# Performance work log

Measured on AMD Instinct MI355X. Metric: run time of the kernel, lower is better.

## Reference

```python
import jax, jax.numpy as jnp
import numpy as np

B, XDIM, TWIN, INCH = 1024, 62, 10, 128
MID, OUT, K, K1, LIN, HC = 256, 512, 3, 10, 512, 4
EPS = 1e-5

REGIONS = [
    list(range(0, 5)),
    list(range(5, 8)) + list(range(14, 17)),
    list(range(8, 11)) + list(range(17, 20)),
    list(range(11, 14)) + list(range(20, 23)),
    list(range(23, 26)) + list(range(32, 35)),
    list(range(26, 29)) + list(range(35, 38)),
    list(range(29, 32)) + list(range(38, 41)),
    list(range(41, 44)) + list(range(50, 52)) + list(range(57, 58)),
    list(range(44, 47)) + list(range(52, 55)) + list(range(58, 61)),
    list(range(47, 50)) + list(range(55, 57)) + list(range(61, 62)),
]


def setup_inputs() -> dict:
    key = jax.random.key(0)
    ks = jax.random.split(key, 40)
    n = lambda k, s, sc=0.02: jax.random.normal(k, s, jnp.float32) * sc
    inp = {
        "x": jax.random.normal(ks[0], (B, XDIM, TWIN, INCH), jnp.float32),
        "tfe_w": n(ks[1], (XDIM, TWIN)),          # depthwise Conv2d (10,1) weight, squeezed
        "tfe_b": jnp.zeros((XDIM,), jnp.float32),
        "cheby1_w": n(ks[2], (K, INCH, OUT)),
        "A": n(ks[3], (XDIM, XDIM)),
        "cheby2_w": n(ks[4], (K, MID, OUT)),
        "A1": n(ks[5], (K1, K1)),
        "b_gate": jnp.float32(1.0),
        "c_gate": jnp.float32(1.0),
        "region_b": jnp.zeros((K1, MID), jnp.float32),
        "hc_w1": n(ks[6], (OUT * 72, LIN)),
        "hc_b1": jnp.zeros((LIN,), jnp.float32),
        "bn1_g": jnp.ones((LIN,), jnp.float32),
        "bn1_b": jnp.zeros((LIN,), jnp.float32),
        "hc_w2": n(ks[7], (LIN, LIN // 2)),
        "hc_b2": jnp.zeros((LIN // 2,), jnp.float32),
        "bn2_g": jnp.ones((LIN // 2,), jnp.float32),
        "bn2_b": jnp.zeros((LIN // 2,), jnp.float32),
        "hc_w3": n(ks[8], (LIN // 2, HC)),
        "hc_b3": jnp.zeros((HC,), jnp.float32),
    }
    for i, idx in enumerate(REGIONS):
        inp[f"rw{i+1}"] = n(ks[10 + i], (MID, INCH, len(idx)))
    return inp


def _cheby(x, L, Ws):
    # sum_k  S_k @ x @ W_k  with S_0 = I, S_k = S_{k-1} @ L ; then ReLU
    S = jnp.eye(L.shape[0], dtype=x.dtype)
    res = jnp.zeros(x.shape[:2] + (Ws.shape[-1],), x.dtype)
    for k in range(Ws.shape[0]):
        res = res + jnp.einsum("nm,bmt,to->bno", S, x, Ws[k])
        S = S @ L
    return jax.nn.relu(res)


def _bn(h, g, b):
    mu = h.mean(axis=0)
    v = h.var(axis=0)  # biased, training-mode BatchNorm1d
    return (h - mu) * jax.lax.rsqrt(v + EPS) * g + b


def _forward(x, tfe_w, tfe_b, cheby1_w, A, cheby2_w, A1, b_gate, c_gate,
             rw1, rw2, rw3, rw4, rw5, rw6, rw7, rw8, rw9, rw10, region_b,
             hc_w1, hc_b1, bn1_g, bn1_b, hc_w2, hc_b2, bn2_g, bn2_b, hc_w3, hc_b3):
    # variance gate (torch.var default: unbiased)
    sigma = jnp.var(x, axis=2, ddof=1)                              # (B, 62, INCH)
    g_tfe = jnp.einsum("bcit,ci->bct", x, tfe_w) + tfe_b[None, :, None]
    g = g_tfe * jnp.exp(-sigma)                                      # (B, 62, INCH)

    g1 = _cheby(g, A, cheby1_w)                                      # (B, 62, OUT)

    rws = [rw1, rw2, rw3, rw4, rw5, rw6, rw7, rw8, rw9, rw10]
    RG = []
    for i, (idx, w) in enumerate(zip(REGIONS, rws)):
        reg = g[:, jnp.asarray(idx), :]                              # (B, L, INCH)
        RG.append(jnp.einsum("blc,mcl->bm", reg, w) + region_b[i])   # Conv1d, full-width kernel
    g2in = jnp.stack(RG, axis=1)                                     # (B, 10, MID)
    g2 = _cheby(g2in, A1, cheby2_w)                                  # (B, 10, OUT)

    att = jnp.concatenate([b_gate * g1, c_gate * g2], axis=1)        # (B, 72, OUT)
    cat = jnp.concatenate([g1, g2], axis=1)
    out = jax.nn.softmax(att, axis=1) * cat
    out = out.reshape(out.shape[0], -1)                              # (B, 72*OUT)

    h = jax.nn.gelu(_bn(out @ hc_w1 + hc_b1, bn1_g, bn1_b), approximate=False)
    h = jax.nn.gelu(_bn(h @ hc_w2 + hc_b2, bn2_g, bn2_b), approximate=False)
    h = h @ hc_w3 + hc_b3
    return jax.nn.softmax(h, axis=1)


def reference(x, tfe_w, tfe_b, cheby1_w, A, cheby2_w, A1, b_gate, c_gate,
              rw1, rw2, rw3, rw4, rw5, rw6, rw7, rw8, rw9, rw10, region_b,
              hc_w1, hc_b1, bn1_g, bn1_b, hc_w2, hc_b2, bn2_g, bn2_b, hc_w3, hc_b3):
    return _forward(x, tfe_w, tfe_b, cheby1_w, A, cheby2_w, A1, b_gate, c_gate,
                    rw1, rw2, rw3, rw4, rw5, rw6, rw7, rw8, rw9, rw10, region_b,
                    hc_w1, hc_b1, bn1_g, bn1_b, hc_w2, hc_b2, bn2_g, bn2_b, hc_w3, hc_b3)
```

## Files before the change

### kernel.cpp

```cpp
#include <hip/hip_runtime.h>
#include <math.h>


__constant__ int cOrder[62] = {
  0,1,2,3,4,
  5,6,7,14,15,16,
  8,9,10,17,18,19,
  11,12,13,20,21,22,
  23,24,25,32,33,34,
  26,27,28,35,36,37,
  29,30,31,38,39,40,
  41,42,43,50,51,57,
  44,45,46,52,53,54,58,59,60,
  47,48,49,55,56,61
};
__constant__ int cPos[62] = {
  0,1,2,3,4, 5,6,7, 11,12,13, 17,18,19, 8,9,10, 14,15,16, 20,21,22,
  23,24,25, 29,30,31, 35,36,37, 26,27,28, 32,33,34, 38,39,40,
  41,42,43, 47,48,49, 56,57,58, 44,45, 50,51,52, 59,60, 46, 53,54,55, 61
};
__constant__ int cRegK[10]   = {640,768,768,768,768,768,768,768,1152,768};
__constant__ int cRegCum[10] = {0,640,1408,2176,2944,3712,4480,5248,6016,7168};

struct Ptr10 { const float* p[10]; };

typedef __attribute__((ext_vector_type(8))) short bf16x8;
typedef __attribute__((ext_vector_type(4))) float f32x4;

__device__ __forceinline__ float gelu_exact(float v){
  return 0.5f * v * (1.0f + erff(v * 0.70710678118654752f));
}
__device__ __forceinline__ unsigned short f2bf(float f){
  unsigned u = __float_as_uint(f);
  unsigned r = (u + 0x7fffu + ((u >> 16) & 1u)) >> 16;
  return (unsigned short)r;
}
__device__ __forceinline__ float bf2f(unsigned short u){
  return __uint_as_float(((unsigned)u) << 16);
}
__device__ __forceinline__ void load_lds16(const unsigned short* g, unsigned short* l){
  __builtin_amdgcn_global_load_lds(
      (const __attribute__((address_space(1))) void*)g,
      (__attribute__((address_space(3))) void*)l, 16, 0, 0);
}

template<bool RELU>
__global__ __launch_bounds__(256) void k_mfma(
    const unsigned short* __restrict__ A, long lda,
    const unsigned short* __restrict__ BT, long ldb,
    void* __restrict__ Cv, int ldc, int kPerZ, long cStrideZ, int mcCount){
  __shared__ unsigned short As[128*32];
  __shared__ unsigned short Bs[128*32];
  int mt, nt, zt;
  if (mcCount){
    int id = blockIdx.x;
    int c = ((id >> 6) << 3) + (id & 7);
    int member = (id >> 3) & 7;
    zt = c / mcCount;
    int mc = c - zt*mcCount;
    mt = mc*2 + (member >> 2);
    nt = member & 3;
  } else { mt = blockIdx.x; nt = blockIdx.y; zt = blockIdx.z; }
  int tid = threadIdx.x;
  int wave = tid >> 6, lane = tid & 63;
  int m0 = mt * 128, n0 = nt * 128;
  int kStart = zt * kPerZ;
  int waveM = wave >> 1, waveN = wave & 1;
  int lr = lane >> 2, ch = lane & 3;
  int quad = lane >> 4, mrow = lane & 15;
  int swe = ((quad ^ (mrow & 3)) << 3);

  int rA0 = wave*32 + lr;
  int rA1 = rA0 + 16;
  int ce  = ((ch ^ (rA0 & 3)) << 3);
  const unsigned short* gA0 = A  + (long)(m0 + rA0)*lda + kStart + ce;
  const unsigned short* gA1 = A  + (long)(m0 + rA1)*lda + kStart + ce;
  const unsigned short* gB0 = BT + (long)(n0 + rA0)*ldb + kStart + ce;
  const unsigned short* gB1 = BT + (long)(n0 + rA1)*ldb + kStart + ce;
  unsigned short* lA0 = &As[(wave*32)*32];
  unsigned short* lA1 = &As[(wave*32+16)*32];
  unsigned short* lB0 = &Bs[(wave*32)*32];
  unsigned short* lB1 = &Bs[(wave*32+16)*32];

  f32x4 acc[4][4] = {};
  int nIter = kPerZ >> 5;
  for (int it = 0; it < nIter; ++it){
    long ko = (long)it << 5;
    load_lds16(gA0 + ko, lA0);
    load_lds16(gA1 + ko, lA1);
    load_lds16(gB0 + ko, lB0);
    load_lds16(gB1 + ko, lB1);
    __syncthreads();
    bf16x8 af[4], bfr[4];
#pragma unroll
    for (int mi = 0; mi < 4; mi++)
      af[mi] = *(const bf16x8*)&As[(waveM*64 + mi*16 + mrow)*32 + swe];
#pragma unroll
    for (int ni = 0; ni < 4; ni++)
      bfr[ni] = *(const bf16x8*)&Bs[(waveN*64 + ni*16 + mrow)*32 + swe];
#pragma unroll
    for (int mi = 0; mi < 4; mi++)
#pragma unroll
      for (int ni = 0; ni < 4; ni++)
        acc[mi][ni] = __builtin_amdgcn_mfma_f32_16x16x32_bf16(
            af[mi], bfr[ni], acc[mi][ni], 0, 0, 0);
    __syncthreads();
  }
  if (RELU){
    unsigned short* C = (unsigned short*)Cv;
#pragma unroll
    for (int mi = 0; mi < 4; mi++)
#pragma unroll
      for (int ni = 0; ni < 4; ni++){
        int col = n0 + waveN*64 + ni*16 + mrow;
#pragma unroll
        for (int r = 0; r < 4; r++){
          int row = m0 + waveM*64 + mi*16 + quad*4 + r;
          C[(long)row*ldc + col] = f2bf(fmaxf(acc[mi][ni][r], 0.f));
        }
      }
  } else {
    float* C = (float*)Cv + (long)zt * cStrideZ;
#pragma unroll
    for (int mi = 0; mi < 4; mi++)
#pragma unroll
      for (int ni = 0; ni < 4; ni++){
        int col = n0 + waveN*64 + ni*16 + mrow;
#pragma unroll
        for (int r = 0; r < 4; r++){
          int row = m0 + waveM*64 + mi*16 + quad*4 + r;
          C[(long)row*ldc + col] = acc[mi][ni][r];
        }
      }
  }
}
template __global__ void k_mfma<true>(const unsigned short*, long, const unsigned short*, long, void*, int, int, long, int);
template __global__ void k_mfma<false>(const unsigned short*, long, const unsigned short*, long, void*, int, int, long, int);

__global__ __launch_bounds__(256) void k_mfma_region(
    const unsigned short* __restrict__ ARb,
    const unsigned short* __restrict__ RWT,
    const float* __restrict__ regb, float* __restrict__ g2in){
  __shared__ unsigned short As[128*32];
  __shared__ unsigned short Bs[128*32];
  int z = blockIdx.z;
  int K = cRegK[z];
  int cumk = cRegCum[z];
  const unsigned short* A  = ARb + cumk;
  const unsigned short* BT = RWT + (long)cumk*256;
  long lda = 7936, ldb = K;
  int tid = threadIdx.x;
  int wave = tid >> 6, lane = tid & 63;
  int m0 = blockIdx.x * 128, n0 = blockIdx.y * 128;
  int waveM = wave >> 1, waveN = wave & 1;
  int lr = lane >> 2, ch = lane & 3;
  int quad = lane >> 4, mrow = lane & 15;
  int swe = ((quad ^ (mrow & 3)) << 3);

  int rA0 = wave*32 + lr;
  int rA1 = rA0 + 16;
  int ce  = ((ch ^ (rA0 & 3)) << 3);
  const unsigned short* gA0 = A  + (long)(m0 + rA0)*lda + ce;
  const unsigned short* gA1 = A  + (long)(m0 + rA1)*lda + ce;
  const unsigned short* gB0 = BT + (long)(n0 + rA0)*ldb + ce;
  const unsigned short* gB1 = BT + (long)(n0 + rA1)*ldb + ce;
  unsigned short* lA0 = &As[(wave*32)*32];
  unsigned short* lA1 = &As[(wave*32+16)*32];
  unsigned short* lB0 = &Bs[(wave*32)*32];
  unsigned short* lB1 = &Bs[(wave*32+16)*32];

  f32x4 acc[4][4] = {};
  int nIter = K >> 5;
  for (int it = 0; it < nIter; ++it){
    long ko = (long)it << 5;
    load_lds16(gA0 + ko, lA0);
    load_lds16(gA1 + ko, lA1);
    load_lds16(gB0 + ko, lB0);
    load_lds16(gB1 + ko, lB1);
    __syncthreads();
    bf16x8 af[4], bfr[4];
#pragma unroll
    for (int mi = 0; mi < 4; mi++)
      af[mi] = *(const bf16x8*)&As[(waveM*64 + mi*16 + mrow)*32 + swe];
#pragma unroll
    for (int ni = 0; ni < 4; ni++)
      bfr[ni] = *(const bf16x8*)&Bs[(waveN*64 + ni*16 + mrow)*32 + swe];
#pragma unroll
    for (int mi = 0; mi < 4; mi++)
#pragma unroll
      for (int ni = 0; ni < 4; ni++)
        acc[mi][ni] = __builtin_amdgcn_mfma_f32_16x16x32_bf16(
            af[mi], bfr[ni], acc[mi][ni], 0, 0, 0);
    __syncthreads();
  }
#pragma unroll
  for (int mi = 0; mi < 4; mi++)
#pragma unroll
    for (int ni = 0; ni < 4; ni++){
      int col = n0 + waveN*64 + ni*16 + mrow;
      float bias = regb[z*256 + col];
#pragma unroll
      for (int r = 0; r < 4; r++){
        int row = m0 + waveM*64 + mi*16 + quad*4 + r;
        g2in[(long)row*2560 + z*256 + col] = acc[mi][ni][r] + bias;
      }
    }
}

__global__ __launch_bounds__(256) void k_prep_all(
    const float* __restrict__ s0, unsigned short* __restrict__ d0,
    const float* __restrict__ s1, unsigned short* __restrict__ d1,
    const float* __restrict__ s2, unsigned short* __restrict__ d2,
    const float* __restrict__ s3, unsigned short* __restrict__ d3,
    Ptr10 rws, unsigned short* __restrict__ RWT,
    const float* __restrict__ Amat, float* __restrict__ AT,
    float* __restrict__ A2T){
  __shared__ float smem[64*65];
  int id = blockIdx.x;
  int tid = threadIdx.x;
  if (id < 7344 && id >= 4784){
    int q = id - 4784;
    int z = q >> 8, m = q & 255;
    int K = cRegK[z], L = K >> 7;
    const float* rw = rws.p[z] + (long)m*K;
    unsigned short* dst = RWT + (long)cRegCum[z]*256 + (long)m*K;
    for (int i = tid; i < K; i += 256) smem[i] = rw[i];
    __syncthreads();
    for (int k = tid; k < K; k += 256){
      int l = k >> 7, c = k & 127;
      dst[k] = f2bf(smem[c*L + l]);
    }
    return;
  }
  if (id >= 7344){
    int r = id - 7344, c = tid;
    if (c < 62) smem[c] = Amat[r*62 + c];
    __syncthreads();
    if (c < 62){
      AT[c*62 + r] = smem[c];
      float s = 0.f;
      for (int t = 0; t < 62; t++) s = fmaf(smem[t], Amat[t*62 + c], s);
      A2T[c*62 + r] = s;
    }
    return;
  }
  const float* src; unsigned short* dst; int R, C, rt, ct;
  if (id < 4608){ src=s0; dst=d0; R=36864; C=512; rt=id>>3;  ct=id&7; }
  else if (id < 4640){ int q=id-4608; src=s1; dst=d1; R=512; C=256; rt=q>>2; ct=q&3; }
  else if (id < 4688){ int q=id-4640; src=s2; dst=d2; R=384; C=512; rt=q>>3; ct=q&7; }
  else { int q=id-4688; src=s3; dst=d3; R=768; C=512; rt=q>>3; ct=q&7; }
  int r0 = rt*64, c0 = ct*64;
  int rr = tid >> 2, cb = (tid & 3) << 2;
#pragma unroll
  for (int i = 0; i < 4; i++){
    int cc = cb + i*16;
    float4 v = *(const float4*)(src + (long)(r0+rr)*C + c0 + cc);
    smem[rr*65+cc+0]=v.x; smem[rr*65+cc+1]=v.y;
    smem[rr*65+cc+2]=v.z; smem[rr*65+cc+3]=v.w;
  }
  __syncthreads();
  int cc = tid >> 2, rb = (tid & 3) << 2;
#pragma unroll
  for (int i = 0; i < 4; i++){
    int r = rb + i*16;
    ushort4 u = make_ushort4(f2bf(smem[(r+0)*65+cc]), f2bf(smem[(r+1)*65+cc]),
                             f2bf(smem[(r+2)*65+cc]), f2bf(smem[(r+3)*65+cc]));
    *(ushort4*)(dst + (long)(c0+cc)*R + r0 + r) = u;
  }
}

__global__ __launch_bounds__(128) void k_g(
    const float* __restrict__ x, const float* __restrict__ tw,
    const float* __restrict__ tb, unsigned short* __restrict__ arb,
    unsigned short* __restrict__ xcat){
  int bid = blockIdx.x;
  int b = bid / 62, n = bid - b*62;
  int t = threadIdx.x;
  const float* xp = x + (long)bid * 1280 + t;
  float s = 0.f, s2 = 0.f, gv = 0.f;
#pragma unroll
  for (int i = 0; i < 10; i++){
    float v = xp[(long)i*128];
    s += v; s2 = fmaf(v, v, s2);
    gv = fmaf(v, tw[n*10 + i], gv);
  }
  float mean = s * 0.1f;
  float var  = (s2 - 10.f*mean*mean) * (1.f/9.f);
  float res  = (gv + tb[n]) * expf(-var);
  unsigned short rb = f2bf(res);
  arb[(long)b*7936 + cPos[n]*128 + t] = rb;
  xcat[(long)b*23808 + n*384 + t]     = rb;
}

__global__ __launch_bounds__(256) void k_spread2(
    const unsigned short* __restrict__ ARb, const float* __restrict__ AT,
    const float* __restrict__ A2T, unsigned short* __restrict__ xcat){
  __shared__ float sgn[7936];
  int b = blockIdx.x, tid = threadIdx.x;
  for (int i = tid; i < 7936; i += 256){
    int p = i >> 7, c = i & 127;
    sgn[cOrder[p]*128 + c] = bf2f(ARb[(long)b*7936 + i]);
  }
  __syncthreads();
  int c = tid & 127, mat = tid >> 7;
  const float* MT = mat ? A2T : AT;
  float acc[62];
#pragma unroll
  for (int n = 0; n < 62; n++) acc[n] = 0.f;
  for (int m = 0; m < 62; m++){
    float gv = sgn[m*128 + c];
    const float* Mp = MT + m*62;
#pragma unroll
    for (int n = 0; n < 62; n++) acc[n] = fmaf(Mp[n], gv, acc[n]);
  }
  long base = (long)b*23808 + (mat+1)*128 + c;
#pragma unroll
  for (int n = 0; n < 62; n++) xcat[base + (long)n*384] = f2bf(acc[n]);
}

__global__ __launch_bounds__(256) void k_x2cat(
    const float* __restrict__ g2in, const float* __restrict__ A1,
    unsigned short* __restrict__ X2){
  __shared__ float sg[2560];
  __shared__ float sA1[100];
  __shared__ float sA2[100];
  int b = blockIdx.x, tid = threadIdx.x;
  for (int i = tid; i < 2560; i += 256) sg[i] = g2in[(long)b*2560 + i];
  if (tid < 100) sA1[tid] = A1[tid];
  __syncthreads();
  if (tid < 100){
    int n = tid/10, m = tid - n*10;
    float a = 0.f;
#pragma unroll
    for (int t = 0; t < 10; t++) a = fmaf(sA1[n*10+t], sA1[t*10+m], a);
    sA2[tid] = a;
  }
  __syncthreads();
  for (int i = tid; i < 2560; i += 256){
    int n = i >> 8, t = i & 255;
    float v1 = 0.f, v2 = 0.f;
#pragma unroll
    for (int m = 0; m < 10; m++){
      float gv = sg[(m<<8) + t];
      v1 = fmaf(sA1[n*10+m], gv, v1);
      v2 = fmaf(sA2[n*10+m], gv, v2);
    }
    long base = (long)b*7680 + n*768;
    X2[base + t]       = f2bf(sg[i]);
    X2[base + 256 + t] = f2bf(v1);
    X2[base + 512 + t] = f2bf(v2);
  }
}

__global__ __launch_bounds__(128) void k_softcat(
    const unsigned short* __restrict__ g1, const unsigned short* __restrict__ g2,
    const float* __restrict__ bg_, const float* __restrict__ cg_,
    unsigned short* __restrict__ outb){
  __shared__ float sc[72][128];
  int b = blockIdx.x;
  int oq = blockIdx.y * 128;
  int tid = threadIdx.x;
  int o = oq + tid;
#pragma unroll
  for (int j = 0; j < 62; j++) sc[j][tid] = bf2f(g1[((long)b*62 + j)*512 + o]);
#pragma unroll
  for (int j = 0; j < 10; j++) sc[62+j][tid] = bf2f(g2[((long)b*10 + j)*512 + o]);
  __syncthreads();
  float bg = *bg_, cg = *cg_;
  float mx = -1e30f;
#pragma unroll
  for (int j = 0; j < 72; j++){
    float av = (j < 62 ? bg : cg) * sc[j][tid];
    mx = fmaxf(mx, av);
  }
  float sum = 0.f;
#pragma unroll
  for (int j = 0; j < 72; j++){
    float v = sc[j][tid];
    float e = expf((j < 62 ? bg : cg) * v - mx);
    sum += e;
    sc[j][tid] = e * v;
  }
  float inv = 1.f / sum;
#pragma unroll
  for (int j = 0; j < 72; j++)
    outb[(long)b*36864 + j*512 + o] = f2bf(sc[j][tid] * inv);
}

__global__ __launch_bounds__(256) void k_reduce(
    const float4* __restrict__ P, float4* __restrict__ h1){
  int idx = blockIdx.x*256 + threadIdx.x;
  float4 v = make_float4(0.f,0.f,0.f,0.f);
#pragma unroll
  for (int s = 0; s < 16; s++){
    float4 p = P[(long)s*131072 + idx];
    v.x += p.x; v.y += p.y; v.z += p.z; v.w += p.w;
  }
  h1[idx] = v;
}

template<int N>
__global__ __launch_bounds__(256) void k_stats(
    const float* __restrict__ h, float* __restrict__ mu, float* __restrict__ rs){
  __shared__ float ls[256], ls2[256];
  int j0 = blockIdx.x * 8;
  int jj = threadIdx.x & 7, bg = threadIdx.x >> 3;
  float s = 0.f, s2 = 0.f;
#pragma unroll 4
  for (int it = 0; it < 32; it++){
    float v = h[(long)(it*32 + bg)*N + j0 + jj];
    s += v; s2 = fmaf(v, v, s2);
  }
  ls[threadIdx.x] = s; ls2[threadIdx.x] = s2;
  __syncthreads();
  if (threadIdx.x < 8){
    float a = ls[threadIdx.x], a2 = ls2[threadIdx.x];
    for (int g = 1; g < 32; g++){ a += ls[g*8 + threadIdx.x]; a2 += ls2[g*8 + threadIdx.x]; }
    float m = a * (1.f/1024.f);
    float var = a2 * (1.f/1024.f) - m*m;
    mu[j0 + threadIdx.x] = m;
    rs[j0 + threadIdx.x] = rsqrtf(var + 1e-5f);
  }
}

__global__ __launch_bounds__(256) void k_bngelu(
    const float* __restrict__ h1, const float* __restrict__ mu,
    const float* __restrict__ rs, const float* __restrict__ gam,
    const float* __restrict__ bet, unsigned short* __restrict__ h1b){
  int base = (blockIdx.x*256 + threadIdx.x) * 4;
  int j = base & 511;
  float4 v = *(const float4*)(h1 + base);
  ushort4 u;
  u.x = f2bf(gelu_exact((v.x - mu[j+0])*rs[j+0]*gam[j+0] + bet[j+0]));
  u.y = f2bf(gelu_exact((v.y - mu[j+1])*rs[j+1]*gam[j+1] + bet[j+1]));
  u.z = f2bf(gelu_exact((v.z - mu[j+2])*rs[j+2]*gam[j+2] + bet[j+2]));
  u.w = f2bf(gelu_exact((v.w - mu[j+3])*rs[j+3]*gam[j+3] + bet[j+3]));
  *(ushort4*)(h1b + base) = u;
}

__global__ __launch_bounds__(256) void k_final(
    const float* __restrict__ h2, const float* __restrict__ mu,
    const float* __restrict__ rs, const float* __restrict__ gam,
    const float* __restrict__ bet, const float* __restrict__ w3,
    const float* __restrict__ b3, float* __restrict__ outp){
  int b = blockIdx.x, tid = threadIdx.x;
  float v = h2[(long)b*256 + tid];
  v = (v - mu[tid]) * rs[tid] * gam[tid] + bet[tid];
  v = gelu_exact(v);
  float4 w = ((const float4*)w3)[tid];
  float p0 = v*w.x, p1 = v*w.y, p2 = v*w.z, p3 = v*w.w;
#pragma unroll
  for (int o = 32; o > 0; o >>= 1){
    p0 += __shfl_down(p0, o);
    p1 += __shfl_down(p1, o);
    p2 += __shfl_down(p2, o);
    p3 += __shfl_down(p3, o);
  }
  __shared__ float red[4][4];
  int wv = tid >> 6;
  if ((tid & 63) == 0){ red[wv][0]=p0; red[wv][1]=p1; red[wv][2]=p2; red[wv][3]=p3; }
  __syncthreads();
  if (tid == 0){
    float l[4];
#pragma unroll
    for (int c = 0; c < 4; c++)
      l[c] = red[0][c]+red[1][c]+red[2][c]+red[3][c] + b3[c];
    float m = fmaxf(fmaxf(l[0], l[1]), fmaxf(l[2], l[3]));
    float e[4]; float sum = 0.f;
#pragma unroll
    for (int c = 0; c < 4; c++){ e[c] = expf(l[c]-m); sum += e[c]; }
    float inv = 1.f / sum;
#pragma unroll
    for (int c = 0; c < 4; c++) outp[(long)b*4 + c] = e[c]*inv;
  }
}

extern "C" void kernel_launch(void* const* d_in, const int* in_sizes, int n_in,
                              void* d_out, int out_size, void* d_ws, size_t ws_size,
                              hipStream_t stream){
  (void)n_in; (void)out_size; (void)ws_size;
  bool dictOrder = (in_sizes[9] == 2560);
  const float* x     = (const float*)d_in[0];
  const float* tfe_w = (const float*)d_in[1];
  const float* tfe_b = (const float*)d_in[2];
  const float* ch1w  = (const float*)d_in[3];
  const float* Amat  = (const float*)d_in[4];
  const float* ch2w  = (const float*)d_in[5];
  const float* A1mat = (const float*)d_in[6];
  const float* bgate = (const float*)d_in[7];
  const float* cgate = (const float*)d_in[8];
  const float* regb  = (const float*)d_in[dictOrder ? 9 : 19];
  int o = dictOrder ? 0 : 10;
  const float* hc_w1 = (const float*)d_in[10+o];
  const float* bn1g  = (const float*)d_in[12+o];
  const float* bn1b  = (const float*)d_in[13+o];
  const float* hc_w2 = (const float*)d_in[14+o];
  const float* bn2g  = (const float*)d_in[16+o];
  const float* bn2b  = (const float*)d_in[17+o];
  const float* hc_w3 = (const float*)d_in[18+o];
  const float* hc_b3 = (const float*)d_in[19+o];
  Ptr10 rws;
  for (int i = 0; i < 10; i++) rws.p[i] = (const float*)d_in[(dictOrder ? 20 : 9) + i];

  char* Wb = (char*)d_ws;
  unsigned short* ARb   = (unsigned short*)(Wb + 0);
  unsigned short* XCAT  = (unsigned short*)(Wb + 16252928);
  unsigned short* RWT   = (unsigned short*)(Wb + 65011712);
  float*          G2IN  = (float*)(Wb + 69074944);
  unsigned short* X2CAT = (unsigned short*)(Wb + 79560704);
  unsigned short* W1T   = (unsigned short*)(Wb + 95289344);
  unsigned short* WC1T  = (unsigned short*)(Wb + 133038080);
  unsigned short* WC2T  = (unsigned short*)(Wb + 133431296);
  unsigned short* G1    = (unsigned short*)(Wb + 134217728);
  unsigned short* G2    = (unsigned short*)(Wb + 199229440);
  unsigned short* OUTB  = (unsigned short*)(Wb + 0);
  float*          P     = (float*)(Wb + 209715200);
  float*          H1    = (float*)(Wb + 243269632);
  float*          H2    = (float*)(Wb + 245366784);
  float*          MU1   = (float*)(Wb + 246415360);
  float*          RS1   = MU1 + 512;
  float*          MU2   = MU1 + 1024;
  float*          RS2   = MU1 + 1280;
  float*          AT    = (float*)(Wb + 246423552);
  float*          A2T   = (float*)(Wb + 246439040);
  unsigned short* W2T   = (unsigned short*)(Wb + 246454528);
  unsigned short* H1B   = (unsigned short*)(Wb + 246716928);

  k_prep_all<<<7406, 256, 0, stream>>>(hc_w1, W1T, hc_w2, W2T, ch1w, WC1T,
                                       ch2w, WC2T, rws, RWT, Amat, AT, A2T);
  k_g<<<1024*62, 128, 0, stream>>>(x, tfe_w, tfe_b, ARb, XCAT);
  k_spread2<<<1024, 256, 0, stream>>>(ARb, AT, A2T, XCAT);
  k_mfma_region<<<dim3(8,2,10), 256, 0, stream>>>(ARb, RWT, regb, G2IN);
  k_x2cat<<<1024, 256, 0, stream>>>(G2IN, A1mat, X2CAT);
  k_mfma<true><<<320, 256, 0, stream>>>(X2CAT, 768, WC2T, 768, (void*)G2, 512, 768, 0, 40);
  k_mfma<true><<<1984, 256, 0, stream>>>(XCAT, 384, WC1T, 384, (void*)G1, 512, 384, 0, 248);
  k_softcat<<<dim3(1024,4), 128, 0, stream>>>(G1, G2, bgate, cgate, OUTB);
  k_mfma<false><<<512, 256, 0, stream>>>(OUTB, 36864, W1T, 36864, (void*)P, 512, 2304, 524288, 4);
  k_reduce<<<512, 256, 0, stream>>>((const float4*)P, (float4*)H1);
  k_stats<512><<<64, 256, 0, stream>>>(H1, MU1, RS1);
  k_bngelu<<<512, 256, 0, stream>>>(H1, MU1, RS1, bn1g, bn1b, H1B);
  k_mfma<false><<<dim3(8,2,1), 256, 0, stream>>>(H1B, 512, W2T, 512, (void*)H2, 256, 512, 0, 0);
  k_stats<256><<<32, 256, 0, stream>>>(H2, MU2, RS2);
  k_final<<<1024, 256, 0, stream>>>(H2, MU2, RS2, bn2g, bn2b, hc_w3, hc_b3, (float*)d_out);
}
```

Measured before the change: 927.7 us.

## Fuse front-end kernels, merge reduce with BN stats, split-K second GEMM

Folds the temporal feature kernel into the weight-prep launch with float4 loads, and zeroes the BN1 accumulators in the same launch. Moves softcat's staging into registers with wider blocks. Combines the split-K partial reduction with the BN1 statistics through atomics, which removes the separate stats kernel. Splits the second hidden GEMM four ways along K and fuses that reduction into its stats kernel. The aim is fewer launches and fewer passes over global memory. In exchange, the atomics make the float summation order nondeterministic.

```diff
diff --git a/kernel.cpp b/kernel.cpp
--- a/kernel.cpp
+++ b/kernel.cpp
@@ -207,17 +207,54 @@
     }
 }
 
-__global__ __launch_bounds__(256) void k_prep_all(
+__global__ __launch_bounds__(256) void k_front(
     const float* __restrict__ s0, unsigned short* __restrict__ d0,
     const float* __restrict__ s1, unsigned short* __restrict__ d1,
     const float* __restrict__ s2, unsigned short* __restrict__ d2,
     const float* __restrict__ s3, unsigned short* __restrict__ d3,
     Ptr10 rws, unsigned short* __restrict__ RWT,
     const float* __restrict__ Amat, float* __restrict__ AT,
-    float* __restrict__ A2T){
+    float* __restrict__ A2T,
+    const float* __restrict__ x, const float* __restrict__ tw,
+    const float* __restrict__ tb, unsigned short* __restrict__ arb,
+    unsigned short* __restrict__ xcat, float* __restrict__ sumz){
   __shared__ float smem[64*65];
   int id = blockIdx.x;
   int tid = threadIdx.x;
+  if (id >= 15342){
+    *(float4*)(sumz + tid*4) = make_float4(0.f,0.f,0.f,0.f);
+    return;
+  }
+  if (id >= 7406){
+    int q = id - 7406;
+    int r = tid >> 5, j = tid & 31;
+    int idx = q*8 + r;
+    int b = idx / 62, n = idx - b*62;
+    const float4* xp = (const float4*)(x + (long)idx*1280) + j;
+    float sx=0.f,sy=0.f,sz=0.f,sw=0.f;
+    float qx=0.f,qy=0.f,qz=0.f,qw=0.f;
+    float gx=0.f,gy=0.f,gz=0.f,gw=0.f;
+#pragma unroll
+    for (int i = 0; i < 10; i++){
+      float4 v = xp[i*32];
+      float w = tw[n*10+i];
+      sx+=v.x; sy+=v.y; sz+=v.z; sw+=v.w;
+      qx=fmaf(v.x,v.x,qx); qy=fmaf(v.y,v.y,qy);
+      qz=fmaf(v.z,v.z,qz); qw=fmaf(v.w,v.w,qw);
+      gx=fmaf(v.x,w,gx); gy=fmaf(v.y,w,gy);
+      gz=fmaf(v.z,w,gz); gw=fmaf(v.w,w,gw);
+    }
+    float tbn = tb[n];
+    float mx_=sx*0.1f, my_=sy*0.1f, mz_=sz*0.1f, mw_=sw*0.1f;
+    float rx = (gx+tbn)*expf(-(qx-10.f*mx_*mx_)*(1.f/9.f));
+    float ry = (gy+tbn)*expf(-(qy-10.f*my_*my_)*(1.f/9.f));
+    float rz = (gz+tbn)*expf(-(qz-10.f*mz_*mz_)*(1.f/9.f));
+    float rw = (gw+tbn)*expf(-(qw-10.f*mw_*mw_)*(1.f/9.f));
+    ushort4 u = make_ushort4(f2bf(rx), f2bf(ry), f2bf(rz), f2bf(rw));
+    *(ushort4*)(arb  + (long)b*7936  + cPos[n]*128 + j*4) = u;
+    *(ushort4*)(xcat + (long)b*23808 + n*384       + j*4) = u;
+    return;
+  }
   if (id < 7344 && id >= 4784){
     int q = id - 4784;
     int z = q >> 8, m = q & 255;
@@ -269,29 +306,6 @@
   }
 }
 
-__global__ __launch_bounds__(128) void k_g(
-    const float* __restrict__ x, const float* __restrict__ tw,
-    const float* __restrict__ tb, unsigned short* __restrict__ arb,
-    unsigned short* __restrict__ xcat){
-  int bid = blockIdx.x;
-  int b = bid / 62, n = bid - b*62;
-  int t = threadIdx.x;
-  const float* xp = x + (long)bid * 1280 + t;
-  float s = 0.f, s2 = 0.f, gv = 0.f;
-#pragma unroll
-  for (int i = 0; i < 10; i++){
-    float v = xp[(long)i*128];
-    s += v; s2 = fmaf(v, v, s2);
-    gv = fmaf(v, tw[n*10 + i], gv);
-  }
-  float mean = s * 0.1f;
-  float var  = (s2 - 10.f*mean*mean) * (1.f/9.f);
-  float res  = (gv + tb[n]) * expf(-var);
-  unsigned short rb = f2bf(res);
-  arb[(long)b*7936 + cPos[n]*128 + t] = rb;
-  xcat[(long)b*23808 + n*384 + t]     = rb;
-}
-
 __global__ __launch_bounds__(256) void k_spread2(
     const unsigned short* __restrict__ ARb, const float* __restrict__ AT,
     const float* __restrict__ A2T, unsigned short* __restrict__ xcat){
@@ -352,90 +366,122 @@
   }
 }
 
-__global__ __launch_bounds__(128) void k_softcat(
+__global__ __launch_bounds__(256) void k_softcat(
     const unsigned short* __restrict__ g1, const unsigned short* __restrict__ g2,
     const float* __restrict__ bg_, const float* __restrict__ cg_,
     unsigned short* __restrict__ outb){
-  __shared__ float sc[72][128];
   int b = blockIdx.x;
-  int oq = blockIdx.y * 128;
-  int tid = threadIdx.x;
-  int o = oq + tid;
-#pragma unroll
-  for (int j = 0; j < 62; j++) sc[j][tid] = bf2f(g1[((long)b*62 + j)*512 + o]);
-#pragma unroll
-  for (int j = 0; j < 10; j++) sc[62+j][tid] = bf2f(g2[((long)b*10 + j)*512 + o]);
-  __syncthreads();
+  int o = blockIdx.y*256 + threadIdx.x;
+  float v[72];
+  const unsigned short* p1 = g1 + (long)b*62*512 + o;
+#pragma unroll
+  for (int j = 0; j < 62; j++) v[j] = bf2f(p1[j*512]);
+  const unsigned short* p2 = g2 + (long)b*10*512 + o;
+#pragma unroll
+  for (int j = 0; j < 10; j++) v[62+j] = bf2f(p2[j*512]);
   float bg = *bg_, cg = *cg_;
   float mx = -1e30f;
 #pragma unroll
   for (int j = 0; j < 72; j++){
-    float av = (j < 62 ? bg : cg) * sc[j][tid];
+    float av = (j < 62 ? bg : cg) * v[j];
     mx = fmaxf(mx, av);
   }
   float sum = 0.f;
 #pragma unroll
   for (int j = 0; j < 72; j++){
-    float v = sc[j][tid];
-    float e = expf((j < 62 ? bg : cg) * v - mx);
+    float e = expf((j < 62 ? bg : cg) * v[j] - mx);
     sum += e;
-    sc[j][tid] = e * v;
+    v[j] = e * v[j];
   }
   float inv = 1.f / sum;
-#pragma unroll
-  for (int j = 0; j < 72; j++)
-    outb[(long)b*36864 + j*512 + o] = f2bf(sc[j][tid] * inv);
-}
-
-__global__ __launch_bounds__(256) void k_reduce(
-    const float4* __restrict__ P, float4* __restrict__ h1){
-  int idx = blockIdx.x*256 + threadIdx.x;
-  float4 v = make_float4(0.f,0.f,0.f,0.f);
-#pragma unroll
-  for (int s = 0; s < 16; s++){
-    float4 p = P[(long)s*131072 + idx];
-    v.x += p.x; v.y += p.y; v.z += p.z; v.w += p.w;
-  }
-  h1[idx] = v;
-}
-
-template<int N>
-__global__ __launch_bounds__(256) void k_stats(
-    const float* __restrict__ h, float* __restrict__ mu, float* __restrict__ rs){
-  __shared__ float ls[256], ls2[256];
+  unsigned short* op = outb + (long)b*36864 + o;
+#pragma unroll
+  for (int j = 0; j < 72; j++) op[j*512] = f2bf(v[j] * inv);
+}
+
+__global__ __launch_bounds__(256) void k_reduce_stats(
+    const float4* __restrict__ P, float4* __restrict__ h1,
+    float* __restrict__ sum, float* __restrict__ ssq){
+  __shared__ float4 ls[128], ls2[128];
+  int c  = threadIdx.x & 127;
+  int rr = threadIdx.x >> 7;
+  int r0 = blockIdx.x * 8;
+  float4 s1 = make_float4(0.f,0.f,0.f,0.f);
+  float4 s2 = make_float4(0.f,0.f,0.f,0.f);
+#pragma unroll
+  for (int k = 0; k < 4; k++){
+    int row = r0 + rr + 2*k;
+    long idx = (long)row*128 + c;
+    float4 v = make_float4(0.f,0.f,0.f,0.f);
+#pragma unroll
+    for (int s = 0; s < 16; s++){
+      float4 p = P[(long)s*131072 + idx];
+      v.x += p.x; v.y += p.y; v.z += p.z; v.w += p.w;
+    }
+    h1[idx] = v;
+    s1.x += v.x; s1.y += v.y; s1.z += v.z; s1.w += v.w;
+    s2.x = fmaf(v.x,v.x,s2.x); s2.y = fmaf(v.y,v.y,s2.y);
+    s2.z = fmaf(v.z,v.z,s2.z); s2.w = fmaf(v.w,v.w,s2.w);
+  }
+  if (rr){ ls[c] = s1; ls2[c] = s2; }
+  __syncthreads();
+  if (!rr){
+    float4 o1 = ls[c], o2 = ls2[c];
+    atomicAdd(&sum[c*4+0], s1.x+o1.x); atomicAdd(&sum[c*4+1], s1.y+o1.y);
+    atomicAdd(&sum[c*4+2], s1.z+o1.z); atomicAdd(&sum[c*4+3], s1.w+o1.w);
+    atomicAdd(&ssq[c*4+0], s2.x+o2.x); atomicAdd(&ssq[c*4+1], s2.y+o2.y);
+    atomicAdd(&ssq[c*4+2], s2.z+o2.z); atomicAdd(&ssq[c*4+3], s2.w+o2.w);
+  }
+}
+
+__global__ __launch_bounds__(256) void k_bngelu(
+    const float* __restrict__ h1, const float* __restrict__ sum,
+    const float* __restrict__ ssq, const float* __restrict__ gam,
+    const float* __restrict__ bet, unsigned short* __restrict__ h1b){
+  int base = (blockIdx.x*256 + threadIdx.x) * 4;
+  int j = base & 511;
+  float4 v = *(const float4*)(h1 + base);
+  float mu0 = sum[j+0]*(1.f/1024.f), mu1 = sum[j+1]*(1.f/1024.f);
+  float mu2 = sum[j+2]*(1.f/1024.f), mu3 = sum[j+3]*(1.f/1024.f);
+  float rs0 = rsqrtf(ssq[j+0]*(1.f/1024.f) - mu0*mu0 + 1e-5f);
+  float rs1 = rsqrtf(ssq[j+1]*(1.f/1024.f) - mu1*mu1 + 1e-5f);
+  float rs2 = rsqrtf(ssq[j+2]*(1.f/1024.f) - mu2*mu2 + 1e-5f);
+  float rs3 = rsqrtf(ssq[j+3]*(1.f/1024.f) - mu3*mu3 + 1e-5f);
+  ushort4 u;
+  u.x = f2bf(gelu_exact((v.x - mu0)*rs0*gam[j+0] + bet[j+0]));
+  u.y = f2bf(gelu_exact((v.y - mu1)*rs1*gam[j+1] + bet[j+1]));
+  u.z = f2bf(gelu_exact((v.z - mu2)*rs2*gam[j+2] + bet[j+2]));
+  u.w = f2bf(gelu_exact((v.w - mu3)*rs3*gam[j+3] + bet[j+3]));
+  *(ushort4*)(h1b + base) = u;
+}
+
+__global__ __launch_bounds__(256) void k_stats2r(
+    const float* __restrict__ P2, float* __restrict__ h2,
+    float* __restrict__ mu, float* __restrict__ rs){
+  __shared__ float lsm[256], lss[256];
   int j0 = blockIdx.x * 8;
   int jj = threadIdx.x & 7, bg = threadIdx.x >> 3;
   float s = 0.f, s2 = 0.f;
 #pragma unroll 4
   for (int it = 0; it < 32; it++){
-    float v = h[(long)(it*32 + bg)*N + j0 + jj];
+    int row = it*32 + bg;
+    float v = 0.f;
+#pragma unroll
+    for (int sp = 0; sp < 4; sp++)
+      v += P2[((long)sp*1024 + row)*256 + j0 + jj];
+    h2[(long)row*256 + j0 + jj] = v;
     s += v; s2 = fmaf(v, v, s2);
   }
-  ls[threadIdx.x] = s; ls2[threadIdx.x] = s2;
+  lsm[threadIdx.x] = s; lss[threadIdx.x] = s2;
   __syncthreads();
   if (threadIdx.x < 8){
-    float a = ls[threadIdx.x], a2 = ls2[threadIdx.x];
-    for (int g = 1; g < 32; g++){ a += ls[g*8 + threadIdx.x]; a2 += ls2[g*8 + threadIdx.x]; }
+    float a = lsm[threadIdx.x], a2 = lss[threadIdx.x];
+    for (int g = 1; g < 32; g++){ a += lsm[g*8 + threadIdx.x]; a2 += lss[g*8 + threadIdx.x]; }
     float m = a * (1.f/1024.f);
     float var = a2 * (1.f/1024.f) - m*m;
     mu[j0 + threadIdx.x] = m;
     rs[j0 + threadIdx.x] = rsqrtf(var + 1e-5f);
   }
-}
-
-__global__ __launch_bounds__(256) void k_bngelu(
-    const float* __restrict__ h1, const float* __restrict__ mu,
-    const float* __restrict__ rs, const float* __restrict__ gam,
-    const float* __restrict__ bet, unsigned short* __restrict__ h1b){
-  int base = (blockIdx.x*256 + threadIdx.x) * 4;
-  int j = base & 511;
-  float4 v = *(const float4*)(h1 + base);
-  ushort4 u;
-  u.x = f2bf(gelu_exact((v.x - mu[j+0])*rs[j+0]*gam[j+0] + bet[j+0]));
-  u.y = f2bf(gelu_exact((v.y - mu[j+1])*rs[j+1]*gam[j+1] + bet[j+1]));
-  u.z = f2bf(gelu_exact((v.z - mu[j+2])*rs[j+2]*gam[j+2] + bet[j+2]));
-  u.w = f2bf(gelu_exact((v.w - mu[j+3])*rs[j+3]*gam[j+3] + bet[j+3]));
-  *(ushort4*)(h1b + base) = u;
 }
 
 __global__ __launch_bounds__(256) void k_final(
@@ -517,29 +563,28 @@
   float*          P     = (float*)(Wb + 209715200);
   float*          H1    = (float*)(Wb + 243269632);
   float*          H2    = (float*)(Wb + 245366784);
-  float*          MU1   = (float*)(Wb + 246415360);
-  float*          RS1   = MU1 + 512;
-  float*          MU2   = MU1 + 1024;
-  float*          RS2   = MU1 + 1280;
+  float*          SUM1  = (float*)(Wb + 246415360);
+  float*          SSQ1  = SUM1 + 512;
+  float*          MU2   = SUM1 + 1024;
+  float*          RS2   = SUM1 + 1280;
   float*          AT    = (float*)(Wb + 246423552);
   float*          A2T   = (float*)(Wb + 246439040);
   unsigned short* W2T   = (unsigned short*)(Wb + 246454528);
   unsigned short* H1B   = (unsigned short*)(Wb + 246716928);
 
-  k_prep_all<<<7406, 256, 0, stream>>>(hc_w1, W1T, hc_w2, W2T, ch1w, WC1T,
-                                       ch2w, WC2T, rws, RWT, Amat, AT, A2T);
-  k_g<<<1024*62, 128, 0, stream>>>(x, tfe_w, tfe_b, ARb, XCAT);
+  k_front<<<15343, 256, 0, stream>>>(hc_w1, W1T, hc_w2, W2T, ch1w, WC1T,
+                                     ch2w, WC2T, rws, RWT, Amat, AT, A2T,
+                                     x, tfe_w, tfe_b, ARb, XCAT, SUM1);
   k_spread2<<<1024, 256, 0, stream>>>(ARb, AT, A2T, XCAT);
   k_mfma_region<<<dim3(8,2,10), 256, 0, stream>>>(ARb, RWT, regb, G2IN);
   k_x2cat<<<1024, 256, 0, stream>>>(G2IN, A1mat, X2CAT);
   k_mfma<true><<<320, 256, 0, stream>>>(X2CAT, 768, WC2T, 768, (void*)G2, 512, 768, 0, 40);
   k_mfma<true><<<1984, 256, 0, stream>>>(XCAT, 384, WC1T, 384, (void*)G1, 512, 384, 0, 248);
-  k_softcat<<<dim3(1024,4), 128, 0, stream>>>(G1, G2, bgate, cgate, OUTB);
+  k_softcat<<<dim3(1024,2), 256, 0, stream>>>(G1, G2, bgate, cgate, OUTB);
   k_mfma<false><<<512, 256, 0, stream>>>(OUTB, 36864, W1T, 36864, (void*)P, 512, 2304, 524288, 4);
-  k_reduce<<<512, 256, 0, stream>>>((const float4*)P, (float4*)H1);
-  k_stats<512><<<64, 256, 0, stream>>>(H1, MU1, RS1);
-  k_bngelu<<<512, 256, 0, stream>>>(H1, MU1, RS1, bn1g, bn1b, H1B);
-  k_mfma<false><<<dim3(8,2,1), 256, 0, stream>>>(H1B, 512, W2T, 512, (void*)H2, 256, 512, 0, 0);
-  k_stats<256><<<32, 256, 0, stream>>>(H2, MU2, RS2);
+  k_reduce_stats<<<128, 256, 0, stream>>>((const float4*)P, (float4*)H1, SUM1, SSQ1);
+  k_bngelu<<<512, 256, 0, stream>>>(H1, SUM1, SSQ1, bn1g, bn1b, H1B);
+  k_mfma<false><<<dim3(8,2,4), 256, 0, stream>>>(H1B, 512, W2T, 512, (void*)P, 256, 128, 262144, 0);
+  k_stats2r<<<32, 256, 0, stream>>>(P, H2, MU2, RS2);
   k_final<<<1024, 256, 0, stream>>>(H2, MU2, RS2, bn2g, bn2b, hc_w3, hc_b3, (float*)d_out);
 }
```

After: 917.1 us. About the same (-1.1%).
